# Kernel optimization log

Measured on AMD Instinct MI355X. Metric: run time of the kernel, lower is better.

## Reference

```python
import jax, jax.numpy as jnp
import numpy as np

B, S, E, H = 64, 197, 768, 12
HD = E // H  # 64


def setup_inputs() -> dict:
    key = jax.random.key(0)
    ks = jax.random.split(key, 9)
    sd = 0.02
    return {
        "x": jax.random.normal(ks[0], (B, S, E), dtype=jnp.float32),
        "Wq": jax.random.normal(ks[1], (E, E), dtype=jnp.float32) * sd,
        "bq": jax.random.normal(ks[2], (E,), dtype=jnp.float32) * sd,
        "Wk": jax.random.normal(ks[3], (E, E), dtype=jnp.float32) * sd,
        "bk": jax.random.normal(ks[4], (E,), dtype=jnp.float32) * sd,
        "Wv": jax.random.normal(ks[5], (E, E), dtype=jnp.float32) * sd,
        "bv": jax.random.normal(ks[6], (E,), dtype=jnp.float32) * sd,
        "Wp": jax.random.normal(ks[7], (E, E), dtype=jnp.float32) * sd,
        "bp": jax.random.normal(ks[8], (E,), dtype=jnp.float32) * sd,
    }


def reference(x, Wq, bq, Wk, bk, Wv, bv, Wp, bp):
    # nn.Linear: y = x @ W.T + b
    Q = x @ Wq.T + bq
    K = x @ Wk.T + bk
    V = x @ Wv.T + bv
    # Faithful to original: plain view (reshape) WITHOUT transpose.
    # (B, S, E) -> (B, H, S, HD): heads index contiguous chunks of the
    # flattened (S*E) memory, exactly as torch .view does.
    Q = Q.reshape(B, H, S, HD)
    K = K.reshape(B, H, S, HD)
    V = V.reshape(B, H, S, HD)
    energy = jnp.einsum("bhqd,bhkd->bhqk", Q, K)  # [B,H,S,S]
    scale = jnp.float32(E) ** 0.5
    # Faithful quirk: softmax FIRST, then divide by sqrt(emb_size).
    att = jax.nn.softmax(energy, axis=-1) / scale
    out = jnp.einsum("bhqk,bhkd->bhqd", att, V)  # [B,H,S,HD]
    out = out.reshape(B, S, E)
    return out @ Wp.T + bp
```

## Files before the change

### kernel.cpp

```cpp
#include <hip/hip_runtime.h>
#include <stdint.h>

#define BSZ 64
#define SEQ 197
#define EMB 768
#define NH  12
#define HD  64
#define M_TOK (BSZ*SEQ)
#define SHD (SEQ*HD)

using bf16x8 = __attribute__((ext_vector_type(8))) short;
using f32x4  = __attribute__((ext_vector_type(4))) float;

__device__ __forceinline__ float bflo(uint32_t u) { return __uint_as_float(u << 16); }
__device__ __forceinline__ uint16_t f2bf(float f) {
    uint32_t u = __float_as_uint(f);
    u += 0x7fffu + ((u >> 16) & 1u);
    return (uint16_t)(u >> 16);
}

struct CvtJob { const float* src; uint16_t* dst; int n8; };
struct CvtJobs { CvtJob j[9]; };

__global__ __launch_bounds__(256) void convert_kernel(CvtJobs jobs)
{
    int idx = blockIdx.x * 256 + threadIdx.x;
    #pragma unroll
    for (int r = 0; r < 9; ++r) {
        const int n8 = jobs.j[r].n8;
        if (idx < n8) {
            const uint4* s4 = (const uint4*)(jobs.j[r].src + (size_t)idx * 8);
            uint4 a = s4[0], b = s4[1];
            uint4 w;
            w.x = (uint32_t)f2bf(__uint_as_float(a.x)) | ((uint32_t)f2bf(__uint_as_float(a.y)) << 16);
            w.y = (uint32_t)f2bf(__uint_as_float(a.z)) | ((uint32_t)f2bf(__uint_as_float(a.w)) << 16);
            w.z = (uint32_t)f2bf(__uint_as_float(b.x)) | ((uint32_t)f2bf(__uint_as_float(b.y)) << 16);
            w.w = (uint32_t)f2bf(__uint_as_float(b.z)) | ((uint32_t)f2bf(__uint_as_float(b.w)) << 16);
            *(uint4*)(jobs.j[r].dst + (size_t)idx * 8) = w;
            return;
        }
        idx -= n8;
    }
}

struct GemmPtrs {
    const uint16_t* W[3];
    const uint16_t* b[3];
    void*           out[3];
};

__global__ __launch_bounds__(256) void gemm_bias_nt(const uint16_t* __restrict__ A,
                                                    GemmPtrs p, int M, int outf32)
{
    __shared__ __align__(16) uint16_t sA[128 * 32];
    __shared__ __align__(16) uint16_t sB[128 * 32];

    const int z = blockIdx.z;
    const uint16_t* __restrict__ W    = p.W[z];
    const uint16_t* __restrict__ bias = p.b[z];

    const int m0   = blockIdx.x * 128;
    const int n0   = blockIdx.y * 128;
    const int tid  = threadIdx.x;
    const int lane = tid & 63;
    const int wave = tid >> 6;
    const int wr = wave >> 1, wc = wave & 1;
    const int l15 = lane & 15;
    const int kq  = lane >> 4;

    const int c0 = tid, c1 = tid + 256;
    const int row0 = c0 >> 2, kc0 = c0 & 3;
    const int row1 = c1 >> 2, kc1 = c1 & 3;
    int ga0 = m0 + row0; if (ga0 >= M) ga0 = M - 1;
    int ga1 = m0 + row1; if (ga1 >= M) ga1 = M - 1;
    const uint16_t* a0p = A + (size_t)ga0 * EMB + kc0 * 8;
    const uint16_t* a1p = A + (size_t)ga1 * EMB + kc1 * 8;
    const uint16_t* b0p = W + (size_t)(n0 + row0) * EMB + kc0 * 8;
    const uint16_t* b1p = W + (size_t)(n0 + row1) * EMB + kc1 * 8;

    f32x4 acc[4][4] = {};

    for (int k0 = 0; k0 < EMB; k0 += 32) {
        __builtin_amdgcn_global_load_lds(
            (const __attribute__((address_space(1))) void*)(a0p + k0),
            (__attribute__((address_space(3))) void*)(sA + c0 * 8), 16, 0, 0);
        __builtin_amdgcn_global_load_lds(
            (const __attribute__((address_space(1))) void*)(a1p + k0),
            (__attribute__((address_space(3))) void*)(sA + c1 * 8), 16, 0, 0);
        __builtin_amdgcn_global_load_lds(
            (const __attribute__((address_space(1))) void*)(b0p + k0),
            (__attribute__((address_space(3))) void*)(sB + c0 * 8), 16, 0, 0);
        __builtin_amdgcn_global_load_lds(
            (const __attribute__((address_space(1))) void*)(b1p + k0),
            (__attribute__((address_space(3))) void*)(sB + c1 * 8), 16, 0, 0);
        asm volatile("s_waitcnt vmcnt(0)" ::: "memory");
        __syncthreads();

        bf16x8 af[4], bfr[4];
        #pragma unroll
        for (int i = 0; i < 4; ++i)
            af[i] = *(const bf16x8*)(sA + (64 * wr + 16 * i + l15) * 32 + kq * 8);
        #pragma unroll
        for (int j = 0; j < 4; ++j)
            bfr[j] = *(const bf16x8*)(sB + (64 * wc + 16 * j + l15) * 32 + kq * 8);

        #pragma unroll
        for (int i = 0; i < 4; ++i)
            #pragma unroll
            for (int j = 0; j < 4; ++j)
                acc[i][j] = __builtin_amdgcn_mfma_f32_16x16x32_bf16(af[i], bfr[j], acc[i][j], 0, 0, 0);

        __syncthreads();
    }

    #pragma unroll
    for (int j = 0; j < 4; ++j) {
        int n = n0 + 64 * wc + 16 * j + l15;
        float bv = bflo((uint32_t)bias[n]);
        #pragma unroll
        for (int i = 0; i < 4; ++i) {
            #pragma unroll
            for (int r = 0; r < 4; ++r) {
                int m = m0 + 64 * wr + 16 * i + kq * 4 + r;
                if (m < M) {
                    float v = acc[i][j][r] + bv;
                    if (outf32) ((float*)p.out[z])[(size_t)m * EMB + n] = v;
                    else        ((uint16_t*)p.out[z])[(size_t)m * EMB + n] = f2bf(v);
                }
            }
        }
    }
}

#define RV 264
#define RP 72
__global__ __launch_bounds__(256) void attn_kernel(const uint16_t* __restrict__ Qg,
                                                   const uint16_t* __restrict__ Kg,
                                                   const uint16_t* __restrict__ Vg,
                                                   uint16_t* __restrict__ Og)
{
    __shared__ __align__(16) uint16_t sVt[HD * RV];
    __shared__ __align__(16) uint16_t sP[4][64 * RP];

    const int bh  = blockIdx.x;
    const size_t base = (size_t)bh * SHD;
    const int tid  = threadIdx.x;
    const int lane = tid & 63;
    const int w    = tid >> 6;
    const int l15  = lane & 15;
    const int kq   = lane >> 4;
    uint16_t* sPw = sP[w];

    {
        int r = tid >> 2, t4 = tid & 3;
        for (int c = SEQ + t4; c < RV; c += 4) sVt[r * RV + c] = 0;
    }
    for (int idx = tid; idx < SHD / 8; idx += 256) {
        int key = idx >> 3, dc = idx & 7;
        uint4 v = ((const uint4*)(Vg + base))[idx];
        uint16_t e[8];
        *(uint4*)e = v;
        #pragma unroll
        for (int j = 0; j < 8; ++j) sVt[(dc * 8 + j) * RV + key] = e[j];
    }

    bf16x8 aq[4][2];
    #pragma unroll
    for (int mi = 0; mi < 4; ++mi) {
        int m = 64 * w + 16 * mi + l15; if (m >= SEQ) m = SEQ - 1;
        const uint16_t* qp = Qg + base + (size_t)m * HD + kq * 8;
        aq[mi][0] = *(const bf16x8*)(qp);
        aq[mi][1] = *(const bf16x8*)(qp + 32);
    }

    bf16x8 ones;
    #pragma unroll
    for (int j = 0; j < 8; ++j) ones[j] = (short)0x3F80;

    f32x4 oacc[4][4] = {};
    f32x4 lacc[4]    = {};

    __syncthreads();

    for (int c = 0; c < 4; ++c) {
        bf16x8 bk[4][2];
        #pragma unroll
        for (int ni = 0; ni < 4; ++ni) {
            int key = 64 * c + 16 * ni + l15; if (key >= SEQ) key = SEQ - 1;
            const uint16_t* kp = Kg + base + (size_t)key * HD + kq * 8;
            bk[ni][0] = *(const bf16x8*)(kp);
            bk[ni][1] = *(const bf16x8*)(kp + 32);
        }
        #pragma unroll
        for (int mi = 0; mi < 4; ++mi) {
            #pragma unroll
            for (int ni = 0; ni < 4; ++ni) {
                f32x4 s = {};
                s = __builtin_amdgcn_mfma_f32_16x16x32_bf16(aq[mi][0], bk[ni][0], s, 0, 0, 0);
                s = __builtin_amdgcn_mfma_f32_16x16x32_bf16(aq[mi][1], bk[ni][1], s, 0, 0, 0);
                int col = 16 * ni + l15;
                int key = 64 * c + col;
                #pragma unroll
                for (int r = 0; r < 4; ++r) {
                    float pv = (key < SEQ) ? __expf(fminf(s[r], 80.f)) : 0.f;
                    sPw[(16 * mi + kq * 4 + r) * RP + col] = f2bf(pv);
                }
            }
        }

        bf16x8 bv[2][4];
        #pragma unroll
        for (int kk = 0; kk < 2; ++kk)
            #pragma unroll
            for (int ni = 0; ni < 4; ++ni)
                bv[kk][ni] = *(const bf16x8*)(sVt + (16 * ni + l15) * RV + c * 64 + kk * 32 + kq * 8);

        #pragma unroll
        for (int mi = 0; mi < 4; ++mi) {
            #pragma unroll
            for (int kk = 0; kk < 2; ++kk) {
                bf16x8 ap = *(const bf16x8*)(sPw + (16 * mi + l15) * RP + kk * 32 + kq * 8);
                lacc[mi] = __builtin_amdgcn_mfma_f32_16x16x32_bf16(ap, ones, lacc[mi], 0, 0, 0);
                #pragma unroll
                for (int ni = 0; ni < 4; ++ni)
                    oacc[mi][ni] = __builtin_amdgcn_mfma_f32_16x16x32_bf16(ap, bv[kk][ni], oacc[mi][ni], 0, 0, 0);
            }
        }
    }

    #pragma unroll
    for (int mi = 0; mi < 4; ++mi) {
        #pragma unroll
        for (int r = 0; r < 4; ++r) {
            int m = 64 * w + 16 * mi + kq * 4 + r;
            if (m < SEQ) {
                float scale = 1.f / (lacc[mi][r] * 27.712812921102035f);
                #pragma unroll
                for (int ni = 0; ni < 4; ++ni)
                    Og[base + (size_t)m * HD + 16 * ni + l15] = f2bf(oacc[mi][ni][r] * scale);
            }
        }
    }
}

extern "C" void kernel_launch(void* const* d_in, const int* in_sizes, int n_in,
                              void* d_out, int out_size, void* d_ws, size_t ws_size,
                              hipStream_t stream)
{
    const size_t NX = (size_t)M_TOK * EMB;
    const size_t NW = (size_t)EMB * EMB;
    const size_t NB = EMB;

    uint16_t* xbf = (uint16_t*)d_ws;
    uint16_t* Wbf[4]; uint16_t* bbf[4];
    uint16_t* cur = xbf + NX;
    for (int i = 0; i < 4; ++i) { Wbf[i] = cur; cur += NW; }
    for (int i = 0; i < 4; ++i) { bbf[i] = cur; cur += NB; }
    uint16_t* Qw = cur;
    uint16_t* Kw = Qw + NX;
    uint16_t* Vw = Kw + NX;

    const size_t need_primary  = 2 * (NX + 4 * NW + 4 * NB + 3 * NX);
    const size_t need_fallback = need_primary - 2 * NX;
    if (ws_size < need_fallback) return;
    if (ws_size < need_primary) Vw = (uint16_t*)d_out;

    CvtJobs jobs;
    jobs.j[0] = { (const float*)d_in[0], xbf,    (int)(NX / 8) };
    jobs.j[1] = { (const float*)d_in[1], Wbf[0], (int)(NW / 8) };
    jobs.j[2] = { (const float*)d_in[3], Wbf[1], (int)(NW / 8) };
    jobs.j[3] = { (const float*)d_in[5], Wbf[2], (int)(NW / 8) };
    jobs.j[4] = { (const float*)d_in[7], Wbf[3], (int)(NW / 8) };
    jobs.j[5] = { (const float*)d_in[2], bbf[0], (int)(NB / 8) };
    jobs.j[6] = { (const float*)d_in[4], bbf[1], (int)(NB / 8) };
    jobs.j[7] = { (const float*)d_in[6], bbf[2], (int)(NB / 8) };
    jobs.j[8] = { (const float*)d_in[8], bbf[3], (int)(NB / 8) };
    const int total8 = (int)((NX + 4 * NW + 4 * NB) / 8);
    convert_kernel<<<(total8 + 255) / 256, 256, 0, stream>>>(jobs);

    GemmPtrs qkv;
    qkv.W[0] = Wbf[0]; qkv.W[1] = Wbf[1]; qkv.W[2] = Wbf[2];
    qkv.b[0] = bbf[0]; qkv.b[1] = bbf[1]; qkv.b[2] = bbf[2];
    qkv.out[0] = Qw; qkv.out[1] = Kw; qkv.out[2] = Vw;
    dim3 g1((M_TOK + 127) / 128, EMB / 128, 3);
    gemm_bias_nt<<<g1, 256, 0, stream>>>(xbf, qkv, M_TOK, 0);

    attn_kernel<<<dim3(BSZ * NH), 256, 0, stream>>>(Qw, Kw, Vw, Qw);

    GemmPtrs pr;
    pr.W[0] = pr.W[1] = pr.W[2] = Wbf[3];
    pr.b[0] = pr.b[1] = pr.b[2] = bbf[3];
    pr.out[0] = pr.out[1] = pr.out[2] = d_out;
    dim3 g2((M_TOK + 127) / 128, EMB / 128, 1);
    gemm_bias_nt<<<g2, 256, 0, stream>>>(Qw, pr, M_TOK, 1);
}
```

Baseline: 274.5 us.

## Double-buffer GEMM LDS tiles and XOR-swizzle k-chunks to avoid bank conflicts

The QKV/projection GEMM now keeps two LDS buffers, so the next k-tile is prefetched with global_load_lds while MFMAs run on the current one, replacing the full load-then-compute serialization. The k-chunk index is also XOR-swizzled by row, both when loading global data into LDS and when reading fragments, to reduce LDS bank conflicts. Shared memory per block doubles, which may lower occupancy, and correctness depends on the hand-written vmcnt/lgkmcnt waits and raw barriers.

New measurement: 276.8 us. About the same (+0.8%).

```diff
diff --git a/kernel.cpp b/kernel.cpp
--- a/kernel.cpp
+++ b/kernel.cpp
@@ -52,8 +52,8 @@
 __global__ __launch_bounds__(256) void gemm_bias_nt(const uint16_t* __restrict__ A,
                                                     GemmPtrs p, int M, int outf32)
 {
-    __shared__ __align__(16) uint16_t sA[128 * 32];
-    __shared__ __align__(16) uint16_t sB[128 * 32];
+    __shared__ __align__(16) uint16_t sA[2][128 * 32];
+    __shared__ __align__(16) uint16_t sB[2][128 * 32];
 
     const int z = blockIdx.z;
     const uint16_t* __restrict__ W    = p.W[z];
@@ -71,38 +71,56 @@
     const int c0 = tid, c1 = tid + 256;
     const int row0 = c0 >> 2, kc0 = c0 & 3;
     const int row1 = c1 >> 2, kc1 = c1 & 3;
+    const int ks0 = (kc0 ^ ((row0 >> 1) & 3)) * 8;
+    const int ks1 = (kc1 ^ ((row1 >> 1) & 3)) * 8;
     int ga0 = m0 + row0; if (ga0 >= M) ga0 = M - 1;
     int ga1 = m0 + row1; if (ga1 >= M) ga1 = M - 1;
-    const uint16_t* a0p = A + (size_t)ga0 * EMB + kc0 * 8;
-    const uint16_t* a1p = A + (size_t)ga1 * EMB + kc1 * 8;
-    const uint16_t* b0p = W + (size_t)(n0 + row0) * EMB + kc0 * 8;
-    const uint16_t* b1p = W + (size_t)(n0 + row1) * EMB + kc1 * 8;
+    const uint16_t* a0p = A + (size_t)ga0 * EMB + ks0;
+    const uint16_t* a1p = A + (size_t)ga1 * EMB + ks1;
+    const uint16_t* b0p = W + (size_t)(n0 + row0) * EMB + ks0;
+    const uint16_t* b1p = W + (size_t)(n0 + row1) * EMB + ks1;
+
+    const int kqs = (kq ^ ((l15 >> 1) & 3)) * 8;
 
     f32x4 acc[4][4] = {};
 
-    for (int k0 = 0; k0 < EMB; k0 += 32) {
-        __builtin_amdgcn_global_load_lds(
-            (const __attribute__((address_space(1))) void*)(a0p + k0),
-            (__attribute__((address_space(3))) void*)(sA + c0 * 8), 16, 0, 0);
-        __builtin_amdgcn_global_load_lds(
-            (const __attribute__((address_space(1))) void*)(a1p + k0),
-            (__attribute__((address_space(3))) void*)(sA + c1 * 8), 16, 0, 0);
-        __builtin_amdgcn_global_load_lds(
-            (const __attribute__((address_space(1))) void*)(b0p + k0),
-            (__attribute__((address_space(3))) void*)(sB + c0 * 8), 16, 0, 0);
-        __builtin_amdgcn_global_load_lds(
-            (const __attribute__((address_space(1))) void*)(b1p + k0),
-            (__attribute__((address_space(3))) void*)(sB + c1 * 8), 16, 0, 0);
-        asm volatile("s_waitcnt vmcnt(0)" ::: "memory");
-        __syncthreads();
+    #define STAGE(buf, k0)                                                        \
+        do {                                                                      \
+            __builtin_amdgcn_global_load_lds(                                     \
+                (const __attribute__((address_space(1))) void*)(a0p + (k0)),      \
+                (__attribute__((address_space(3))) void*)(sA[buf] + c0 * 8), 16, 0, 0); \
+            __builtin_amdgcn_global_load_lds(                                     \
+                (const __attribute__((address_space(1))) void*)(a1p + (k0)),      \
+                (__attribute__((address_space(3))) void*)(sA[buf] + c1 * 8), 16, 0, 0); \
+            __builtin_amdgcn_global_load_lds(                                     \
+                (const __attribute__((address_space(1))) void*)(b0p + (k0)),      \
+                (__attribute__((address_space(3))) void*)(sB[buf] + c0 * 8), 16, 0, 0); \
+            __builtin_amdgcn_global_load_lds(                                     \
+                (const __attribute__((address_space(1))) void*)(b1p + (k0)),      \
+                (__attribute__((address_space(3))) void*)(sB[buf] + c1 * 8), 16, 0, 0); \
+        } while (0)
+
+    STAGE(0, 0);
+
+    const int NIT = EMB / 32;
+    for (int it = 0; it < NIT; ++it) {
+        const int cur = it & 1;
+        if (it + 1 < NIT) {
+            STAGE(cur ^ 1, (it + 1) * 32);
+            asm volatile("s_waitcnt vmcnt(4)" ::: "memory");
+        } else {
+            asm volatile("s_waitcnt vmcnt(0)" ::: "memory");
+        }
+        __builtin_amdgcn_s_barrier();
+        asm volatile("" ::: "memory");
 
         bf16x8 af[4], bfr[4];
         #pragma unroll
         for (int i = 0; i < 4; ++i)
-            af[i] = *(const bf16x8*)(sA + (64 * wr + 16 * i + l15) * 32 + kq * 8);
+            af[i] = *(const bf16x8*)(sA[cur] + (64 * wr + 16 * i + l15) * 32 + kqs);
         #pragma unroll
         for (int j = 0; j < 4; ++j)
-            bfr[j] = *(const bf16x8*)(sB + (64 * wc + 16 * j + l15) * 32 + kq * 8);
+            bfr[j] = *(const bf16x8*)(sB[cur] + (64 * wc + 16 * j + l15) * 32 + kqs);
 
         #pragma unroll
         for (int i = 0; i < 4; ++i)
@@ -110,8 +128,11 @@
             for (int j = 0; j < 4; ++j)
                 acc[i][j] = __builtin_amdgcn_mfma_f32_16x16x32_bf16(af[i], bfr[j], acc[i][j], 0, 0, 0);
 
-        __syncthreads();
-    }
+        asm volatile("s_waitcnt lgkmcnt(0)" ::: "memory");
+        __builtin_amdgcn_s_barrier();
+        asm volatile("" ::: "memory");
+    }
+    #undef STAGE
 
     #pragma unroll
     for (int j = 0; j < 4; ++j) {
```
